# Kernel tuning notes

Measured on AMD Instinct MI355X. Metric: run time of the kernel, lower is better.

The kernel has to match this reference:

```python
import jax, jax.numpy as jnp
import numpy as np

B, T, V, E, D = 64, 512, 512, 128, 256


def setup_inputs() -> dict:
    key = jax.random.key(0)
    ks = jax.random.split(key, 9)
    g = lambda k, sh, s: jax.random.normal(k, sh, jnp.float32) * np.float32(s)
    return {
        "x": jax.random.randint(ks[0], (B, T), 0, V),
        "embed": g(ks[1], (V, E), 1.0),
        "W_ih": g(ks[2], (E, D), 1.0 / np.sqrt(E)),
        "W_hh": g(ks[3], (D, D), 1.0 / np.sqrt(D)),
        "b_h": jnp.zeros((D,), jnp.float32),
        "W_attn": g(ks[4], (D, D), 1.0 / np.sqrt(D)),
        "U_attn": g(ks[5], (D, D), 1.0 / np.sqrt(D)),
        "v_attn": g(ks[6], (D,), 1.0 / np.sqrt(D)),
        "fc_W": g(ks[7], (2 * D, V), 1.0 / np.sqrt(2 * D)),
        "fc_b": jnp.zeros((V,), jnp.float32),
    }


def _forward(x, embed, W_ih, W_hh, b_h, W_attn, U_attn, v_attn, fc_W, fc_b):
    Bn, Tn = x.shape
    Dn = W_hh.shape[0]
    # precompute input projection for every step: [T, B, D]
    xp = jnp.swapaxes(embed[x] @ W_ih + b_h, 0, 1)
    pos = jnp.arange(Tn)

    def step(carry, x_t):
        h_prev, Hbuf, Pbuf, t = carry  # Hbuf: past hidden states, Pbuf: W_attn-projected
        h = jnp.tanh(x_t + h_prev @ W_hh)  # [B, D]
        # Bahdanau attention over strictly-past states (slots < t)
        cur_proj = h @ U_attn  # [B, D]
        energy = jnp.einsum('tbd,d->tb', jnp.tanh(Pbuf + cur_proj[None]), v_attn)
        energy = jnp.where((pos < t)[:, None], energy, -1e9)
        w = jax.nn.softmax(energy, axis=0)  # [T, B]
        ctx = jnp.einsum('tb,tbd->bd', w, Hbuf)
        ctx = jnp.where(t == 0, h, ctx)  # first step: context = h itself
        logits = jnp.concatenate([h, ctx], axis=-1) @ fc_W + fc_b  # [B, V]
        Hbuf = Hbuf.at[t].set(h)
        Pbuf = Pbuf.at[t].set(h @ W_attn)
        return (h, Hbuf, Pbuf, t + 1), logits

    h0 = jnp.zeros((Bn, Dn), xp.dtype)
    buf = jnp.zeros((Tn, Bn, Dn), xp.dtype)
    _, outs = jax.lax.scan(step, (h0, buf, buf, jnp.asarray(0, jnp.int32)), xp)
    return jnp.swapaxes(outs, 0, 1)  # [B, T, V]


def reference(x, embed, W_ih, W_hh, b_h, W_attn, U_attn, v_attn, fc_W, fc_b):
    return _forward(x, embed, W_ih, W_hh, b_h, W_attn, U_attn, v_attn, fc_W, fc_b)
```

## Files before the change

kernel.cpp:

```cpp
#include <hip/hip_runtime.h>
#include <hip/hip_bf16.h>

#define B_  64
#define T_  512
#define V_  512
#define E_  128
#define D_  256
#define D2_ 512

typedef unsigned short u16;
typedef unsigned int   u32;
typedef short s16x8 __attribute__((ext_vector_type(8)));
typedef _Float16 f16x8 __attribute__((ext_vector_type(8)));
typedef float f32x4 __attribute__((ext_vector_type(4)));
typedef unsigned short u16x2 __attribute__((ext_vector_type(2)));
typedef unsigned short u16x4 __attribute__((ext_vector_type(4)));

__device__ __forceinline__ float bf2f(u16 u){
    union { u32 i; float f; } c; c.i = ((u32)u) << 16; return c.f;
}
__device__ __forceinline__ u16 f2bf(float f){
    union { float f; u32 i; } c; c.f = f;
    u32 u = c.i;
    return (u16)((u + 0x7fffu + ((u >> 16) & 1u)) >> 16);
}
__device__ __forceinline__ u16 f2h(float f){
    union { _Float16 h; u16 u; } c; c.h = (_Float16)f; return c.u;
}
__device__ __forceinline__ float tanh_b(float x){
    float e = __expf(2.0f * x);
    return fmaf(-2.0f, __builtin_amdgcn_rcpf(e + 1.0f), 1.0f);
}
__device__ __forceinline__ void barrier_lgkm(){
    asm volatile("s_waitcnt lgkmcnt(0)\n\ts_barrier" ::: "memory");
}

__global__ __launch_bounds__(256) void k_ew_cvt(const float* __restrict__ embed,
                                                const float* __restrict__ W_ih,
                                                const float* __restrict__ b_h,
                                                float* __restrict__ EW,
                                                const float* __restrict__ W_att,
                                                const float* __restrict__ U_att,
                                                const float* __restrict__ fc_W,
                                                u16* __restrict__ Wab,
                                                u16* __restrict__ Uab,
                                                u16* __restrict__ fcWb){
    __shared__ float er[E_];
    int blk = blockIdx.x;
    int tid = threadIdx.x;
    if (blk < V_){
        if (tid < E_) er[tid] = embed[blk*E_ + tid];
        __syncthreads();
        float acc = b_h[tid];
        #pragma unroll 4
        for (int e = 0; e < E_; ++e) acc += er[e] * W_ih[e*D_ + tid];
        EW[blk*D_ + tid] = acc;
    } else {
        int i = (blk - V_) * 256 + tid;
        if (i < 65536){
            int n = i >> 8, k = i & 255;
            Wab[i] = f2bf(W_att[k*D_ + n]);
        } else if (i < 131072){
            int j = i - 65536;
            int n = j >> 8, k = j & 255;
            Uab[j] = f2bf(U_att[k*D_ + n]);
        } else {
            int j = i - 131072;
            int n = j >> 9, k = j & 511;
            fcWb[j] = f2bf(fc_W[k*V_ + n]);
        }
    }
}

__global__ __launch_bounds__(256) void k_gather(const int* __restrict__ x,
                                                const float* __restrict__ EW,
                                                float* __restrict__ XP){
    int m = blockIdx.x * 4 + (threadIdx.x >> 6);
    int lane = threadIdx.x & 63;
    int b = m & 63, t = m >> 6;
    int v = x[b*T_ + t];
    float4 val = *(const float4*)&EW[v*D_ + lane*4];
    *(float4*)&XP[(size_t)m*D_ + lane*4] = val;
}

__global__ __launch_bounds__(512, 2) void k_rnn(const float* __restrict__ XP,
                                                const float* __restrict__ W_hh,
                                                u16* __restrict__ HC){
    __shared__ u16 hf[2][4][272];
    int tid  = threadIdx.x;
    int lane = tid & 63;
    int w    = tid >> 6;
    int col  = lane & 15;
    int colA = col & 3;
    int quad = lane >> 4;
    int bb0  = blockIdx.x * 4;

    f16x8 bfh[2][8];
    #pragma unroll
    for (int nt = 0; nt < 2; ++nt){
        int n = w*32 + nt*16 + col;
        #pragma unroll
        for (int ks = 0; ks < 8; ++ks){
            f16x8 th;
            #pragma unroll
            for (int j = 0; j < 8; ++j){
                int k = ks*32 + quad*8 + j;
                th[j] = (_Float16)W_hh[k*D_ + n];
            }
            bfh[nt][ks] = th;
        }
    }
    for (int i = tid; i < 2*4*272; i += 512) (&hf[0][0][0])[i] = 0;

    const float* p  = XP + (size_t)bb0*D_ + w*32 + col;
    u16*         hc = HC + (size_t)bb0*D2_ + w*32 + col;

    float ewv[2][4];
    #pragma unroll
    for (int nt = 0; nt < 2; ++nt)
        #pragma unroll
        for (int r = 0; r < 4; ++r)
            ewv[nt][r] = p[r*D_ + nt*16];
    p += (size_t)B_*D_;
    __syncthreads();

    for (int t = 0; t < T_; ++t){
        int rb = t & 1, wb = rb ^ 1;
        f32x4 acc[2];
        #pragma unroll
        for (int nt = 0; nt < 2; ++nt)
            #pragma unroll
            for (int r = 0; r < 4; ++r) acc[nt][r] = ewv[nt][r];

        f16x8 ah[8];
        #pragma unroll
        for (int ks = 0; ks < 8; ++ks)
            ah[ks] = *(const f16x8*)&hf[rb][colA][ks*32 + quad*8];

        if (t + 1 < T_){
            #pragma unroll
            for (int nt = 0; nt < 2; ++nt)
                #pragma unroll
                for (int r = 0; r < 4; ++r)
                    ewv[nt][r] = p[r*D_ + nt*16];
        }
        p += (size_t)B_*D_;

        #pragma unroll
        for (int ks = 0; ks < 8; ++ks){
            acc[0] = __builtin_amdgcn_mfma_f32_16x16x32_f16(ah[ks], bfh[0][ks], acc[0], 0, 0, 0);
            acc[1] = __builtin_amdgcn_mfma_f32_16x16x32_f16(ah[ks], bfh[1][ks], acc[1], 0, 0, 0);
        }

        #pragma unroll
        for (int nt = 0; nt < 2; ++nt){
            f32x4 s = acc[nt];
            float v = (quad & 2) ? ((quad & 1) ? s[3] : s[2])
                                 : ((quad & 1) ? s[1] : s[0]);
            float h  = tanh_b(v);
            int n    = w*32 + nt*16 + col;
            hf[wb][quad][n]      = f2h(h);
            hc[quad*D2_ + nt*16] = f2bf(h);
        }
        hc += (size_t)B_*D2_;
        barrier_lgkm();
    }
}

__global__ __launch_bounds__(256) void k_gemm(const u16* __restrict__ A, int lda,
                                              const u16* __restrict__ Wb,
                                              const float* __restrict__ bias,
                                              void* __restrict__ out,
                                              int K, int N, int mode){
    __shared__ u16 As[64][88];
    __shared__ u16 Ws[64][88];
    int tid  = threadIdx.x;
    int lane = tid & 63;
    int w    = tid >> 6;
    int col  = lane & 15;
    int quad = lane >> 4;
    int m0   = blockIdx.x * 64;
    int n0   = blockIdx.y * 64;

    f32x4 acc[4];
    #pragma unroll
    for (int nt = 0; nt < 4; ++nt)
        #pragma unroll
        for (int r = 0; r < 4; ++r) acc[nt][r] = 0.0f;

    for (int kk = 0; kk < K; kk += 64){
        #pragma unroll
        for (int i = 0; i < 2; ++i){
            int idx = tid + i*256;
            int r   = idx >> 3;
            int c8  = (idx & 7) * 8;
            *(s16x8*)&As[r][c8] = *(const s16x8*)&A [(size_t)(m0 + r)*lda + kk + c8];
            *(s16x8*)&Ws[r][c8] = *(const s16x8*)&Wb[(size_t)(n0 + r)*K   + kk + c8];
        }
        barrier_lgkm();
        #pragma unroll
        for (int ks = 0; ks < 2; ++ks){
            s16x8 a = *(const s16x8*)&As[w*16 + col][ks*32 + quad*8];
            #pragma unroll
            for (int nt = 0; nt < 4; ++nt){
                s16x8 b = *(const s16x8*)&Ws[nt*16 + col][ks*32 + quad*8];
                acc[nt] = __builtin_amdgcn_mfma_f32_16x16x32_bf16(a, b, acc[nt], 0, 0, 0);
            }
        }
        barrier_lgkm();
    }
    #pragma unroll
    for (int nt = 0; nt < 4; ++nt){
        int n = n0 + nt*16 + col;
        float bv = (mode == 1 && bias) ? bias[n] : 0.0f;
        #pragma unroll
        for (int r = 0; r < 4; ++r){
            int m = m0 + w*16 + quad*4 + r;
            float v = acc[nt][r] + bv;
            if (mode == 1){
                int b = m & 63, t = m >> 6;
                ((float*)out)[(size_t)(b*T_ + t)*V_ + n] = v;
            } else if (mode == 2){
                ((u16*)out)[(size_t)m*N + n] = f2bf(__expf(2.0f * v));
            } else if (mode == 3){
                u16* dst = (u16*)out + ((size_t)(n >> 8)) * ((size_t)32768 * 256);
                dst[(size_t)m*256 + (n & 255)] = f2bf(__expf(2.0f * v));
            } else {
                ((u16*)out)[(size_t)m*N + n] = f2bf(v);
            }
        }
    }
}

__global__ __launch_bounds__(512) void k_fc(const u16* __restrict__ A,
                                            const u16* __restrict__ Wb,
                                            const float* __restrict__ bias,
                                            float* __restrict__ out){
    __shared__ u16 As[128][88];
    __shared__ u16 Ws[128][88];
    int tid  = threadIdx.x;
    int lane = tid & 63;
    int w    = tid >> 6;
    int wm   = w >> 2;
    int wn   = w & 3;
    int col  = lane & 15;
    int quad = lane >> 4;
    int m0   = blockIdx.x * 128;
    int n0   = blockIdx.y * 128;

    f32x4 acc[4][2];
    #pragma unroll
    for (int mt = 0; mt < 4; ++mt)
        #pragma unroll
        for (int nt = 0; nt < 2; ++nt)
            #pragma unroll
            for (int r = 0; r < 4; ++r) acc[mt][nt][r] = 0.0f;

    for (int kk = 0; kk < D2_; kk += 64){
        #pragma unroll
        for (int i = 0; i < 2; ++i){
            int idx = tid + i*512;
            int r   = idx >> 3;
            int c8  = (idx & 7) * 8;
            *(s16x8*)&As[r][c8] = *(const s16x8*)&A [(size_t)(m0 + r)*D2_ + kk + c8];
            *(s16x8*)&Ws[r][c8] = *(const s16x8*)&Wb[(size_t)(n0 + r)*D2_ + kk + c8];
        }
        barrier_lgkm();
        #pragma unroll
        for (int ks = 0; ks < 2; ++ks){
            s16x8 b0 = *(const s16x8*)&Ws[wn*32 +      col][ks*32 + quad*8];
            s16x8 b1 = *(const s16x8*)&Ws[wn*32 + 16 + col][ks*32 + quad*8];
            #pragma unroll
            for (int mt = 0; mt < 4; ++mt){
                s16x8 a = *(const s16x8*)&As[wm*64 + mt*16 + col][ks*32 + quad*8];
                acc[mt][0] = __builtin_amdgcn_mfma_f32_16x16x32_bf16(a, b0, acc[mt][0], 0, 0, 0);
                acc[mt][1] = __builtin_amdgcn_mfma_f32_16x16x32_bf16(a, b1, acc[mt][1], 0, 0, 0);
            }
        }
        barrier_lgkm();
    }
    #pragma unroll
    for (int nt = 0; nt < 2; ++nt){
        int n = n0 + wn*32 + nt*16 + col;
        float bv = bias[n];
        #pragma unroll
        for (int mt = 0; mt < 4; ++mt){
            #pragma unroll
            for (int r = 0; r < 4; ++r){
                int m = m0 + wm*64 + mt*16 + quad*4 + r;
                int b = m & 63, t = m >> 6;
                out[(size_t)(b*T_ + t)*V_ + n] = acc[mt][nt][r] + bv;
            }
        }
    }
}

__global__ __launch_bounds__(256) void k_energy(const u16* __restrict__ EP,
                                                const u16* __restrict__ EQ,
                                                const float* __restrict__ v_attn,
                                                u16* __restrict__ Wx){
    __shared__ float eps[32][288];
    int tid = threadIdx.x;
    int blk = blockIdx.x;
    int b   = blk / 136;
    int pi  = blk % 136;
    int tt  = 0;
    while ((tt+1)*(tt+2)/2 <= pi) ++tt;
    int pt  = pi - tt*(tt+1)/2;

    int t_l = tid >> 3;
    int dg  = tid & 7;
    int d0  = dg * 32;
    int t   = tt*32 + t_l;

    #pragma unroll
    for (int i = 0; i < 8; ++i){
        int idx = tid + i*256;
        int row = idx >> 6;
        int c4  = (idx & 63) * 4;
        int pc  = c4 + ((c4 >> 5) << 2);
        u16x4 v4 = *(const u16x4*)&EP[((size_t)((pt*32 + row)*B_ + b))*D_ + c4];
        float4 f4 = make_float4(bf2f(v4.x), bf2f(v4.y), bf2f(v4.z), bf2f(v4.w));
        *(float4*)&eps[row][pc] = f4;
    }

    float eq[32], vm2[32], sv = 0.0f;
    #pragma unroll
    for (int i = 0; i < 8; ++i){
        u16x4 v4 = *(const u16x4*)&EQ[((size_t)(t*B_ + b))*D_ + d0 + i*4];
        eq[i*4+0] = bf2f(v4.x); eq[i*4+1] = bf2f(v4.y);
        eq[i*4+2] = bf2f(v4.z); eq[i*4+3] = bf2f(v4.w);
    }
    #pragma unroll
    for (int i = 0; i < 32; ++i){
        float v = v_attn[d0 + i];
        sv += v;
        vm2[i] = -2.0f * v;
    }
    barrier_lgkm();

    for (int tpl = 0; tpl < 32; ++tpl){
        int tp = pt*32 + tpl;
        float acc = sv;
        #pragma unroll
        for (int g = 0; g < 8; ++g){
            float4 ep = *(const float4*)&eps[tpl][dg*36 + 4*g];
            float da = fmaf(ep.x, eq[4*g+0], 1.0f);
            float db = fmaf(ep.y, eq[4*g+1], 1.0f);
            float dc = fmaf(ep.z, eq[4*g+2], 1.0f);
            float dd = fmaf(ep.w, eq[4*g+3], 1.0f);
            float dab = da * db;
            float dcd = dc * dd;
            float nab = fmaf(vm2[4*g+1], da, vm2[4*g+0] * db);
            float ncd = fmaf(vm2[4*g+3], dc, vm2[4*g+2] * dd);
            float num = fmaf(ncd, dab, nab * dcd);
            acc = fmaf(num, __builtin_amdgcn_rcpf(dab * dcd), acc);
        }
        acc += __shfl_xor(acc, 1);
        acc += __shfl_xor(acc, 2);
        acc += __shfl_xor(acc, 4);
        if (dg == 0 && tp < t){
            Wx[((size_t)(b*T_ + t))*T_ + tp] = f2bf(__expf(acc));
        }
    }
}

__global__ __launch_bounds__(256) void k_ctx(const u16* __restrict__ Wx,
                                             u16* __restrict__ HC){
    __shared__ u16 As[64][88];
    __shared__ u16 Ws[64][88];
    __shared__ float rs[64];
    int tid  = threadIdx.x;
    int lane = tid & 63;
    int w    = tid >> 6;
    int col  = lane & 15;
    int quad = lane >> 4;
    int b    = blockIdx.y;
    int m0   = (blockIdx.x >> 2) * 64;
    int n0   = (blockIdx.x & 3) * 64;

    const u16* A = Wx + (size_t)b * T_ * T_;

    int r0 = tid >> 3;
    int c8 = (tid & 7) * 8;
    float rsum0 = 0.0f, rsum1 = 0.0f;

    f32x4 acc[4];
    #pragma unroll
    for (int nt = 0; nt < 4; ++nt)
        #pragma unroll
        for (int r = 0; r < 4; ++r) acc[nt][r] = 0.0f;

    int kmax = m0 + 64;
    for (int kk = 0; kk < kmax; kk += 64){
        bool diag = (kk == m0);
        #pragma unroll
        for (int i = 0; i < 2; ++i){
            int r = r0 + i*32;
            s16x8 v = *(const s16x8*)&A[(size_t)(m0 + r)*T_ + kk + c8];
            if (diag){
                #pragma unroll
                for (int j = 0; j < 8; ++j)
                    if (c8 + j >= r) v[j] = 0;
            }
            *(s16x8*)&As[r][c8] = v;
            float s = 0.0f;
            #pragma unroll
            for (int j = 0; j < 8; ++j) s += bf2f((u16)v[j]);
            if (i == 0) rsum0 += s; else rsum1 += s;
        }
        #pragma unroll
        for (int i = 0; i < 8; ++i){
            int idx = tid + i*256;
            int k   = idx >> 5;
            int n2  = (idx & 31) * 2;
            u16x2 v2 = *(const u16x2*)&HC[((size_t)((kk + k)*B_ + b))*D2_ + n0 + n2];
            Ws[n2][k]   = v2.x;
            Ws[n2+1][k] = v2.y;
        }
        barrier_lgkm();
        #pragma unroll
        for (int ks = 0; ks < 2; ++ks){
            s16x8 a = *(const s16x8*)&As[w*16 + col][ks*32 + quad*8];
            #pragma unroll
            for (int nt = 0; nt < 4; ++nt){
                s16x8 bb = *(const s16x8*)&Ws[nt*16 + col][ks*32 + quad*8];
                acc[nt] = __builtin_amdgcn_mfma_f32_16x16x32_bf16(a, bb, acc[nt], 0, 0, 0);
            }
        }
        barrier_lgkm();
    }

    rsum0 += __shfl_xor(rsum0, 1); rsum0 += __shfl_xor(rsum0, 2); rsum0 += __shfl_xor(rsum0, 4);
    rsum1 += __shfl_xor(rsum1, 1); rsum1 += __shfl_xor(rsum1, 2); rsum1 += __shfl_xor(rsum1, 4);
    if ((tid & 7) == 0){ rs[r0] = rsum0; rs[r0 + 32] = rsum1; }
    barrier_lgkm();

    float linv[4];
    #pragma unroll
    for (int r = 0; r < 4; ++r){
        int rr = w*16 + quad*4 + r;
        float lv = (m0 + rr > 0) ? rs[rr] : 1.0f;
        linv[r] = 1.0f / lv;
    }
    #pragma unroll
    for (int nt = 0; nt < 4; ++nt){
        int n = n0 + nt*16 + col;
        #pragma unroll
        for (int r = 0; r < 4; ++r){
            int t = m0 + w*16 + quad*4 + r;
            u16 ov;
            if (t == 0) ov = HC[(size_t)b*D2_ + n];
            else        ov = f2bf(acc[nt][r] * linv[r]);
            HC[((size_t)(t*B_ + b))*D2_ + D_ + n] = ov;
        }
    }
}

extern "C" void kernel_launch(void* const* d_in, const int* in_sizes, int n_in,
                              void* d_out, int out_size, void* d_ws, size_t ws_size,
                              hipStream_t stream){
    const int*   x     = (const int*)d_in[0];
    const float* embed = (const float*)d_in[1];
    const float* W_ih  = (const float*)d_in[2];
    const float* W_hh  = (const float*)d_in[3];
    const float* b_h   = (const float*)d_in[4];
    const float* W_att = (const float*)d_in[5];
    const float* U_att = (const float*)d_in[6];
    const float* v_att = (const float*)d_in[7];
    const float* fc_W  = (const float*)d_in[8];
    const float* fc_b  = (const float*)d_in[9];

    char* ws = (char*)d_ws;
    float* EW   = (float*)ws;
    u16*   Wab  = (u16*)(ws + 524288);
    u16*   Uab  = (u16*)(ws + 655360);
    u16*   fcWb = (u16*)(ws + 786432);
    u16*   HC   = (u16*)(ws + 1310720);
    u16*   EP   = (u16*)(ws + 34865152);
    u16*   EQ   = (u16*)(ws + 51642368);
    float* XP   = (float*)(ws + 34865152);
    u16*   Wx   = (u16*)d_out;

    k_ew_cvt<<<dim3(2048),        dim3(256), 0, stream>>>(embed, W_ih, b_h, EW,
                                                          W_att, U_att, fc_W,
                                                          Wab, Uab, fcWb);
    k_gather<<<dim3(T_*B_/4),     dim3(256), 0, stream>>>(x, EW, XP);
    k_rnn   <<<dim3(16),          dim3(512), 0, stream>>>(XP, W_hh, HC);
    k_gemm  <<<dim3(512, 8),      dim3(256), 0, stream>>>(HC, D2_, Wab, nullptr, (void*)EP, D_, D2_, 3);
    k_energy<<<dim3(B_*136),      dim3(256), 0, stream>>>(EP, EQ, v_att, Wx);
    k_ctx   <<<dim3(32, B_),      dim3(256), 0, stream>>>(Wx, HC);
    k_fc    <<<dim3(256, 4),      dim3(512), 0, stream>>>(HC, fcWb, fc_b, (float*)d_out);
}
```

Before: 686.0 us.

## Fuse RNN, projection GEMM and energy into persistent mega-kernel with flag sync

The separate RNN, projection GEMM and energy kernels are merged into one persistent kernel. Sixteen blocks run the recurrence and publish progress flags every 8 timesteps. The remaining blocks pull work items from an atomic queue, spin-wait on those flags, and then compute P/Q projection tiles and energy tiles while the serial RNN is still running. The aim is to hide the GEMM and energy work behind the latency-bound recurrence. The cost is spin-wait overhead, reliance on all blocks being co-resident to avoid deadlock, and a workspace/output buffer layout reshuffled to hold the flags.

```diff
diff --git a/kernel.cpp b/kernel.cpp
--- a/kernel.cpp
+++ b/kernel.cpp
@@ -7,6 +7,10 @@
 #define E_  128
 #define D_  256
 #define D2_ 512
+
+#define NPQ    4096
+#define NEN    8704
+#define NITEMS (NPQ + NEN)
 
 typedef unsigned short u16;
 typedef unsigned int   u32;
@@ -41,10 +45,7 @@
                                                 float* __restrict__ EW,
                                                 const float* __restrict__ W_att,
                                                 const float* __restrict__ U_att,
-                                                const float* __restrict__ fc_W,
-                                                u16* __restrict__ Wab,
-                                                u16* __restrict__ Uab,
-                                                u16* __restrict__ fcWb){
+                                                u16* __restrict__ Wab){
     __shared__ float er[E_];
     int blk = blockIdx.x;
     int tid = threadIdx.x;
@@ -60,14 +61,10 @@
         if (i < 65536){
             int n = i >> 8, k = i & 255;
             Wab[i] = f2bf(W_att[k*D_ + n]);
-        } else if (i < 131072){
+        } else {
             int j = i - 65536;
             int n = j >> 8, k = j & 255;
-            Uab[j] = f2bf(U_att[k*D_ + n]);
-        } else {
-            int j = i - 131072;
-            int n = j >> 9, k = j & 511;
-            fcWb[j] = f2bf(fc_W[k*V_ + n]);
+            Wab[i] = f2bf(U_att[k*D_ + n]);
         }
     }
 }
@@ -83,11 +80,20 @@
     *(float4*)&XP[(size_t)m*D_ + lane*4] = val;
 }
 
-__global__ __launch_bounds__(512, 2) void k_rnn(const float* __restrict__ XP,
-                                                const float* __restrict__ W_hh,
-                                                u16* __restrict__ HC){
-    __shared__ u16 hf[2][4][272];
-    int tid  = threadIdx.x;
+__global__ __launch_bounds__(256) void k_cvt_fc(const float* __restrict__ fc_W,
+                                                u16* __restrict__ fcWb){
+    int j = blockIdx.x * 256 + threadIdx.x;
+    int n = j >> 9, k = j & 511;
+    fcWb[j] = f2bf(fc_W[k*V_ + n]);
+}
+
+
+__device__ void rnn_block(const float* __restrict__ XP,
+                          const float* __restrict__ W_hh,
+                          u16* __restrict__ HC,
+                          u32* __restrict__ flags,
+                          char* smem, int tid){
+    u16 (*hf)[4][272] = (u16 (*)[4][272])smem;
     int lane = tid & 63;
     int w    = tid >> 6;
     int col  = lane & 15;
@@ -163,24 +169,214 @@
             hc[quad*D2_ + nt*16] = f2bf(h);
         }
         hc += (size_t)B_*D2_;
+
+        if ((t & 7) == 7){
+            asm volatile("s_waitcnt vmcnt(0) lgkmcnt(0)" ::: "memory");
+            __syncthreads();
+            if (tid == 0)
+                __hip_atomic_fetch_add(&flags[t >> 3], 1u,
+                                       __ATOMIC_RELEASE, __HIP_MEMORY_SCOPE_AGENT);
+        } else {
+            barrier_lgkm();
+        }
+    }
+}
+
+__device__ void pq_tile(int t, int nt, const u16* __restrict__ HC,
+                        const u16* __restrict__ Wab,
+                        u16* __restrict__ EP, u16* __restrict__ EQ,
+                        char* smem, int tid){
+    u16 (*As)[88] = (u16 (*)[88])smem;
+    u16 (*Ws)[88] = (u16 (*)[88])(smem + 64*88*2);
+    int lane = tid & 63;
+    int w  = tid >> 6;
+    int wm = w >> 2, wn = w & 3;
+    int col = lane & 15, quad = lane >> 4;
+    int m0 = t * 64, n0 = nt * 64;
+    int r  = tid >> 3, c8 = (tid & 7) * 8;
+
+    f32x4 acc[2];
+    #pragma unroll
+    for (int mt = 0; mt < 2; ++mt)
+        #pragma unroll
+        for (int rr = 0; rr < 4; ++rr) acc[mt][rr] = 0.0f;
+
+    for (int kk = 0; kk < D_; kk += 64){
+        *(s16x8*)&As[r][c8] = *(const s16x8*)&HC [(size_t)(m0 + r)*D2_ + kk + c8];
+        *(s16x8*)&Ws[r][c8] = *(const s16x8*)&Wab[(size_t)(n0 + r)*D_  + kk + c8];
         barrier_lgkm();
-    }
-}
-
-__global__ __launch_bounds__(256) void k_gemm(const u16* __restrict__ A, int lda,
-                                              const u16* __restrict__ Wb,
-                                              const float* __restrict__ bias,
-                                              void* __restrict__ out,
-                                              int K, int N, int mode){
+        #pragma unroll
+        for (int ks = 0; ks < 2; ++ks){
+            s16x8 b = *(const s16x8*)&Ws[wn*16 + col][ks*32 + quad*8];
+            #pragma unroll
+            for (int mt = 0; mt < 2; ++mt){
+                s16x8 a = *(const s16x8*)&As[wm*32 + mt*16 + col][ks*32 + quad*8];
+                acc[mt] = __builtin_amdgcn_mfma_f32_16x16x32_bf16(a, b, acc[mt], 0, 0, 0);
+            }
+        }
+        barrier_lgkm();
+    }
+    int n = n0 + wn*16 + col;
+    u16* dst = (n < D_) ? EP : EQ;
+    int nn = n & 255;
+    #pragma unroll
+    for (int mt = 0; mt < 2; ++mt)
+        #pragma unroll
+        for (int rr = 0; rr < 4; ++rr){
+            int m = m0 + wm*32 + mt*16 + quad*4 + rr;
+            dst[(size_t)m*D_ + nn] = f2bf(__expf(2.0f * acc[mt][rr]));
+        }
+}
+
+__device__ void energy_tile(int b, int tt, int pt,
+                            const u16* __restrict__ EP, const u16* __restrict__ EQ,
+                            const float* __restrict__ v_attn,
+                            u16* __restrict__ Wx, char* smem, int tid){
+    float (*eps)[288] = (float (*)[288])smem;
+    int tg = tid >> 4, dg = tid & 15;
+    int d0 = dg * 16;
+    int t  = tt*32 + tg;
+
+    #pragma unroll
+    for (int i = 0; i < 4; ++i){
+        int idx = tid + i*512;
+        int row = idx >> 6;
+        int c4  = (idx & 63) * 4;
+        int pc  = c4 + ((c4 >> 5) << 2);
+        u16x4 v4 = *(const u16x4*)&EP[((size_t)((pt*32 + row)*B_ + b))*D_ + c4];
+        *(float4*)&eps[row][pc] = make_float4(bf2f(v4.x), bf2f(v4.y), bf2f(v4.z), bf2f(v4.w));
+    }
+
+    float eq[16], vm2[16], sv = 0.0f;
+    #pragma unroll
+    for (int i = 0; i < 4; ++i){
+        u16x4 v4 = *(const u16x4*)&EQ[((size_t)(t*B_ + b))*D_ + d0 + i*4];
+        eq[i*4+0] = bf2f(v4.x); eq[i*4+1] = bf2f(v4.y);
+        eq[i*4+2] = bf2f(v4.z); eq[i*4+3] = bf2f(v4.w);
+    }
+    #pragma unroll
+    for (int i = 0; i < 16; ++i){
+        float v = v_attn[d0 + i];
+        sv += v;
+        vm2[i] = -2.0f * v;
+    }
+    int po[4];
+    #pragma unroll
+    for (int g = 0; g < 4; ++g){ int c = d0 + 4*g; po[g] = c + ((c >> 5) << 2); }
+    barrier_lgkm();
+
+    for (int tpl = 0; tpl < 32; ++tpl){
+        int tp = pt*32 + tpl;
+        float acc = sv;
+        #pragma unroll
+        for (int g = 0; g < 4; ++g){
+            float4 ep = *(const float4*)&eps[tpl][po[g]];
+            float da = fmaf(ep.x, eq[4*g+0], 1.0f);
+            float db = fmaf(ep.y, eq[4*g+1], 1.0f);
+            float dc = fmaf(ep.z, eq[4*g+2], 1.0f);
+            float dd = fmaf(ep.w, eq[4*g+3], 1.0f);
+            float dab = da * db;
+            float dcd = dc * dd;
+            float nab = fmaf(vm2[4*g+1], da, vm2[4*g+0] * db);
+            float ncd = fmaf(vm2[4*g+3], dc, vm2[4*g+2] * dd);
+            float num = fmaf(ncd, dab, nab * dcd);
+            acc = fmaf(num, __builtin_amdgcn_rcpf(dab * dcd), acc);
+        }
+        acc += __shfl_xor(acc, 1);
+        acc += __shfl_xor(acc, 2);
+        acc += __shfl_xor(acc, 4);
+        acc += __shfl_xor(acc, 8);
+        if (dg == 0 && tp < t)
+            Wx[((size_t)(b*T_ + t))*T_ + tp] = f2bf(__expf(acc));
+    }
+}
+
+__device__ void worker_loop(const u16* __restrict__ HC,
+                            const u16* __restrict__ Wab,
+                            u16* __restrict__ EP, u16* __restrict__ EQ,
+                            const float* __restrict__ v_attn,
+                            u16* __restrict__ Wx,
+                            u32* __restrict__ flags,
+                            char* smem, int tid){
+    volatile int* s_item = (volatile int*)(smem + 36864);
+    for (;;){
+        __syncthreads();
+        if (tid == 0)
+            *s_item = (int)__hip_atomic_fetch_add(&flags[95], 1u,
+                          __ATOMIC_RELAXED, __HIP_MEMORY_SCOPE_AGENT);
+        __syncthreads();
+        int item = *s_item;
+        if (item >= NITEMS) return;
+
+        if (item < NPQ){
+            int t  = item >> 3, nt = item & 7;
+            if (tid == 0){
+                while (__hip_atomic_load(&flags[t >> 3], __ATOMIC_ACQUIRE,
+                                         __HIP_MEMORY_SCOPE_AGENT) < 16u)
+                    __builtin_amdgcn_s_sleep(8);
+            }
+            __syncthreads();
+            pq_tile(t, nt, HC, Wab, EP, EQ, smem, tid);
+            asm volatile("s_waitcnt vmcnt(0)" ::: "memory");
+            __syncthreads();
+            if (tid == 0)
+                __hip_atomic_fetch_add(&flags[64 + (t >> 5)], 1u,
+                                       __ATOMIC_RELEASE, __HIP_MEMORY_SCOPE_AGENT);
+        } else {
+            int e  = item - NPQ;
+            int pi = e >> 6, b = e & 63;
+            int tt = 0;
+            while ((tt+1)*(tt+2)/2 <= pi) ++tt;
+            int pt = pi - tt*(tt+1)/2;
+            if (tid == 0){
+                while (__hip_atomic_load(&flags[64 + tt], __ATOMIC_ACQUIRE,
+                                         __HIP_MEMORY_SCOPE_AGENT) < 256u)
+                    __builtin_amdgcn_s_sleep(8);
+                while (__hip_atomic_load(&flags[64 + pt], __ATOMIC_ACQUIRE,
+                                         __HIP_MEMORY_SCOPE_AGENT) < 256u)
+                    __builtin_amdgcn_s_sleep(8);
+            }
+            __syncthreads();
+            energy_tile(b, tt, pt, EP, EQ, v_attn, Wx, smem, tid);
+        }
+    }
+}
+
+__global__ __launch_bounds__(512, 2) void k_mega(const float* __restrict__ XP,
+                                                 const float* __restrict__ W_hh,
+                                                 u16* __restrict__ HC,
+                                                 const u16* __restrict__ Wab,
+                                                 const float* __restrict__ v_attn,
+                                                 u16* __restrict__ EP,
+                                                 u16* __restrict__ EQ,
+                                                 u16* __restrict__ Wx,
+                                                 u32* __restrict__ flags){
+    __shared__ __align__(16) char smem[36880];
+    int tid = threadIdx.x;
+    if (blockIdx.x < 16)
+        rnn_block(XP, W_hh, HC, flags, smem, tid);
+    worker_loop(HC, Wab, EP, EQ, v_attn, Wx, flags, smem, tid);
+}
+
+__global__ __launch_bounds__(256) void k_ctx(const u16* __restrict__ Wx,
+                                             u16* __restrict__ HC){
     __shared__ u16 As[64][88];
     __shared__ u16 Ws[64][88];
+    __shared__ float rs[64];
     int tid  = threadIdx.x;
     int lane = tid & 63;
     int w    = tid >> 6;
     int col  = lane & 15;
     int quad = lane >> 4;
-    int m0   = blockIdx.x * 64;
-    int n0   = blockIdx.y * 64;
+    int b    = blockIdx.y;
+    int m0   = (blockIdx.x >> 2) * 64;
+    int n0   = (blockIdx.x & 3) * 64;
+
+    const u16* A = Wx + (size_t)b * T_ * T_;
+
+    int r0 = tid >> 3;
+    int c8 = (tid & 7) * 8;
+    float rsum0 = 0.0f, rsum1 = 0.0f;
 
     f32x4 acc[4];
     #pragma unroll
@@ -188,14 +384,32 @@
         #pragma unroll
         for (int r = 0; r < 4; ++r) acc[nt][r] = 0.0f;
 
-    for (int kk = 0; kk < K; kk += 64){
+    int kmax = m0 + 64;
+    for (int kk = 0; kk < kmax; kk += 64){
+        bool diag = (kk == m0);
         #pragma unroll
         for (int i = 0; i < 2; ++i){
+            int r = r0 + i*32;
+            s16x8 v = *(const s16x8*)&A[(size_t)(m0 + r)*T_ + kk + c8];
+            if (diag){
+                #pragma unroll
+                for (int j = 0; j < 8; ++j)
+                    if (c8 + j >= r) v[j] = 0;
+            }
+            *(s16x8*)&As[r][c8] = v;
+            float s = 0.0f;
+            #pragma unroll
+            for (int j = 0; j < 8; ++j) s += bf2f((u16)v[j]);
+            if (i == 0) rsum0 += s; else rsum1 += s;
+        }
+        #pragma unroll
+        for (int i = 0; i < 8; ++i){
             int idx = tid + i*256;
-            int r   = idx >> 3;
-            int c8  = (idx & 7) * 8;
-            *(s16x8*)&As[r][c8] = *(const s16x8*)&A [(size_t)(m0 + r)*lda + kk + c8];
-            *(s16x8*)&Ws[r][c8] = *(const s16x8*)&Wb[(size_t)(n0 + r)*K   + kk + c8];
+            int k   = idx >> 5;
+            int n2  = (idx & 31) * 2;
+            u16x2 v2 = *(const u16x2*)&HC[((size_t)((kk + k)*B_ + b))*D2_ + n0 + n2];
+            Ws[n2][k]   = v2.x;
+            Ws[n2+1][k] = v2.y;
         }
         barrier_lgkm();
         #pragma unroll
@@ -203,31 +417,35 @@
             s16x8 a = *(const s16x8*)&As[w*16 + col][ks*32 + quad*8];
             #pragma unroll
             for (int nt = 0; nt < 4; ++nt){
-                s16x8 b = *(const s16x8*)&Ws[nt*16 + col][ks*32 + quad*8];
-                acc[nt] = __builtin_amdgcn_mfma_f32_16x16x32_bf16(a, b, acc[nt], 0, 0, 0);
+                s16x8 bb = *(const s16x8*)&Ws[nt*16 + col][ks*32 + quad*8];
+                acc[nt] = __builtin_amdgcn_mfma_f32_16x16x32_bf16(a, bb, acc[nt], 0, 0, 0);
             }
         }
         barrier_lgkm();
+    }
+
+    rsum0 += __shfl_xor(rsum0, 1); rsum0 += __shfl_xor(rsum0, 2); rsum0 += __shfl_xor(rsum0, 4);
+    rsum1 += __shfl_xor(rsum1, 1); rsum1 += __shfl_xor(rsum1, 2); rsum1 += __shfl_xor(rsum1, 4);
+    if ((tid & 7) == 0){ rs[r0] = rsum0; rs[r0 + 32] = rsum1; }
+    barrier_lgkm();
+
+    float linv[4];
+    #pragma unroll
+    for (int r = 0; r < 4; ++r){
+        int rr = w*16 + quad*4 + r;
+        float lv = (m0 + rr > 0) ? rs[rr] : 1.0f;
+        linv[r] = 1.0f / lv;
     }
     #pragma unroll
     for (int nt = 0; nt < 4; ++nt){
         int n = n0 + nt*16 + col;
-        float bv = (mode == 1 && bias) ? bias[n] : 0.0f;
         #pragma unroll
         for (int r = 0; r < 4; ++r){
-            int m = m0 + w*16 + quad*4 + r;
-            float v = acc[nt][r] + bv;
-            if (mode == 1){
-                int b = m & 63, t = m >> 6;
-                ((float*)out)[(size_t)(b*T_ + t)*V_ + n] = v;
-            } else if (mode == 2){
-                ((u16*)out)[(size_t)m*N + n] = f2bf(__expf(2.0f * v));
-            } else if (mode == 3){
-                u16* dst = (u16*)out + ((size_t)(n >> 8)) * ((size_t)32768 * 256);
-                dst[(size_t)m*256 + (n & 255)] = f2bf(__expf(2.0f * v));
-            } else {
-                ((u16*)out)[(size_t)m*N + n] = f2bf(v);
-            }
+            int t = m0 + w*16 + quad*4 + r;
+            u16 ov;
+            if (t == 0) ov = HC[(size_t)b*D2_ + n];
+            else        ov = f2bf(acc[nt][r] * linv[r]);
+            HC[((size_t)(t*B_ + b))*D2_ + D_ + n] = ov;
         }
     }
 }
@@ -295,168 +513,6 @@
     }
 }
 
-__global__ __launch_bounds__(256) void k_energy(const u16* __restrict__ EP,
-                                                const u16* __restrict__ EQ,
-                                                const float* __restrict__ v_attn,
-                                                u16* __restrict__ Wx){
-    __shared__ float eps[32][288];
-    int tid = threadIdx.x;
-    int blk = blockIdx.x;
-    int b   = blk / 136;
-    int pi  = blk % 136;
-    int tt  = 0;
-    while ((tt+1)*(tt+2)/2 <= pi) ++tt;
-    int pt  = pi - tt*(tt+1)/2;
-
-    int t_l = tid >> 3;
-    int dg  = tid & 7;
-    int d0  = dg * 32;
-    int t   = tt*32 + t_l;
-
-    #pragma unroll
-    for (int i = 0; i < 8; ++i){
-        int idx = tid + i*256;
-        int row = idx >> 6;
-        int c4  = (idx & 63) * 4;
-        int pc  = c4 + ((c4 >> 5) << 2);
-        u16x4 v4 = *(const u16x4*)&EP[((size_t)((pt*32 + row)*B_ + b))*D_ + c4];
-        float4 f4 = make_float4(bf2f(v4.x), bf2f(v4.y), bf2f(v4.z), bf2f(v4.w));
-        *(float4*)&eps[row][pc] = f4;
-    }
-
-    float eq[32], vm2[32], sv = 0.0f;
-    #pragma unroll
-    for (int i = 0; i < 8; ++i){
-        u16x4 v4 = *(const u16x4*)&EQ[((size_t)(t*B_ + b))*D_ + d0 + i*4];
-        eq[i*4+0] = bf2f(v4.x); eq[i*4+1] = bf2f(v4.y);
-        eq[i*4+2] = bf2f(v4.z); eq[i*4+3] = bf2f(v4.w);
-    }
-    #pragma unroll
-    for (int i = 0; i < 32; ++i){
-        float v = v_attn[d0 + i];
-        sv += v;
-        vm2[i] = -2.0f * v;
-    }
-    barrier_lgkm();
-
-    for (int tpl = 0; tpl < 32; ++tpl){
-        int tp = pt*32 + tpl;
-        float acc = sv;
-        #pragma unroll
-        for (int g = 0; g < 8; ++g){
-            float4 ep = *(const float4*)&eps[tpl][dg*36 + 4*g];
-            float da = fmaf(ep.x, eq[4*g+0], 1.0f);
-            float db = fmaf(ep.y, eq[4*g+1], 1.0f);
-            float dc = fmaf(ep.z, eq[4*g+2], 1.0f);
-            float dd = fmaf(ep.w, eq[4*g+3], 1.0f);
-            float dab = da * db;
-            float dcd = dc * dd;
-            float nab = fmaf(vm2[4*g+1], da, vm2[4*g+0] * db);
-            float ncd = fmaf(vm2[4*g+3], dc, vm2[4*g+2] * dd);
-            float num = fmaf(ncd, dab, nab * dcd);
-            acc = fmaf(num, __builtin_amdgcn_rcpf(dab * dcd), acc);
-        }
-        acc += __shfl_xor(acc, 1);
-        acc += __shfl_xor(acc, 2);
-        acc += __shfl_xor(acc, 4);
-        if (dg == 0 && tp < t){
-            Wx[((size_t)(b*T_ + t))*T_ + tp] = f2bf(__expf(acc));
-        }
-    }
-}
-
-__global__ __launch_bounds__(256) void k_ctx(const u16* __restrict__ Wx,
-                                             u16* __restrict__ HC){
-    __shared__ u16 As[64][88];
-    __shared__ u16 Ws[64][88];
-    __shared__ float rs[64];
-    int tid  = threadIdx.x;
-    int lane = tid & 63;
-    int w    = tid >> 6;
-    int col  = lane & 15;
-    int quad = lane >> 4;
-    int b    = blockIdx.y;
-    int m0   = (blockIdx.x >> 2) * 64;
-    int n0   = (blockIdx.x & 3) * 64;
-
-    const u16* A = Wx + (size_t)b * T_ * T_;
-
-    int r0 = tid >> 3;
-    int c8 = (tid & 7) * 8;
-    float rsum0 = 0.0f, rsum1 = 0.0f;
-
-    f32x4 acc[4];
-    #pragma unroll
-    for (int nt = 0; nt < 4; ++nt)
-        #pragma unroll
-        for (int r = 0; r < 4; ++r) acc[nt][r] = 0.0f;
-
-    int kmax = m0 + 64;
-    for (int kk = 0; kk < kmax; kk += 64){
-        bool diag = (kk == m0);
-        #pragma unroll
-        for (int i = 0; i < 2; ++i){
-            int r = r0 + i*32;
-            s16x8 v = *(const s16x8*)&A[(size_t)(m0 + r)*T_ + kk + c8];
-            if (diag){
-                #pragma unroll
-                for (int j = 0; j < 8; ++j)
-                    if (c8 + j >= r) v[j] = 0;
-            }
-            *(s16x8*)&As[r][c8] = v;
-            float s = 0.0f;
-            #pragma unroll
-            for (int j = 0; j < 8; ++j) s += bf2f((u16)v[j]);
-            if (i == 0) rsum0 += s; else rsum1 += s;
-        }
-        #pragma unroll
-        for (int i = 0; i < 8; ++i){
-            int idx = tid + i*256;
-            int k   = idx >> 5;
-            int n2  = (idx & 31) * 2;
-            u16x2 v2 = *(const u16x2*)&HC[((size_t)((kk + k)*B_ + b))*D2_ + n0 + n2];
-            Ws[n2][k]   = v2.x;
-            Ws[n2+1][k] = v2.y;
-        }
-        barrier_lgkm();
-        #pragma unroll
-        for (int ks = 0; ks < 2; ++ks){
-            s16x8 a = *(const s16x8*)&As[w*16 + col][ks*32 + quad*8];
-            #pragma unroll
-            for (int nt = 0; nt < 4; ++nt){
-                s16x8 bb = *(const s16x8*)&Ws[nt*16 + col][ks*32 + quad*8];
-                acc[nt] = __builtin_amdgcn_mfma_f32_16x16x32_bf16(a, bb, acc[nt], 0, 0, 0);
-            }
-        }
-        barrier_lgkm();
-    }
-
-    rsum0 += __shfl_xor(rsum0, 1); rsum0 += __shfl_xor(rsum0, 2); rsum0 += __shfl_xor(rsum0, 4);
-    rsum1 += __shfl_xor(rsum1, 1); rsum1 += __shfl_xor(rsum1, 2); rsum1 += __shfl_xor(rsum1, 4);
-    if ((tid & 7) == 0){ rs[r0] = rsum0; rs[r0 + 32] = rsum1; }
-    barrier_lgkm();
-
-    float linv[4];
-    #pragma unroll
-    for (int r = 0; r < 4; ++r){
-        int rr = w*16 + quad*4 + r;
-        float lv = (m0 + rr > 0) ? rs[rr] : 1.0f;
-        linv[r] = 1.0f / lv;
-    }
-    #pragma unroll
-    for (int nt = 0; nt < 4; ++nt){
-        int n = n0 + nt*16 + col;
-        #pragma unroll
-        for (int r = 0; r < 4; ++r){
-            int t = m0 + w*16 + quad*4 + r;
-            u16 ov;
-            if (t == 0) ov = HC[(size_t)b*D2_ + n];
-            else        ov = f2bf(acc[nt][r] * linv[r]);
-            HC[((size_t)(t*B_ + b))*D2_ + D_ + n] = ov;
-        }
-    }
-}
-
 extern "C" void kernel_launch(void* const* d_in, const int* in_sizes, int n_in,
                               void* d_out, int out_size, void* d_ws, size_t ws_size,
                               hipStream_t stream){
@@ -473,22 +529,25 @@
 
     char* ws = (char*)d_ws;
     float* EW   = (float*)ws;
+    u16*   fcWb = (u16*)ws;
     u16*   Wab  = (u16*)(ws + 524288);
-    u16*   Uab  = (u16*)(ws + 655360);
-    u16*   fcWb = (u16*)(ws + 786432);
-    u16*   HC   = (u16*)(ws + 1310720);
-    u16*   EP   = (u16*)(ws + 34865152);
-    u16*   EQ   = (u16*)(ws + 51642368);
-    float* XP   = (float*)(ws + 34865152);
-    u16*   Wx   = (u16*)d_out;
-
-    k_ew_cvt<<<dim3(2048),        dim3(256), 0, stream>>>(embed, W_ih, b_h, EW,
-                                                          W_att, U_att, fc_W,
-                                                          Wab, Uab, fcWb);
-    k_gather<<<dim3(T_*B_/4),     dim3(256), 0, stream>>>(x, EW, XP);
-    k_rnn   <<<dim3(16),          dim3(512), 0, stream>>>(XP, W_hh, HC);
-    k_gemm  <<<dim3(512, 8),      dim3(256), 0, stream>>>(HC, D2_, Wab, nullptr, (void*)EP, D_, D2_, 3);
-    k_energy<<<dim3(B_*136),      dim3(256), 0, stream>>>(EP, EQ, v_att, Wx);
-    k_ctx   <<<dim3(32, B_),      dim3(256), 0, stream>>>(Wx, HC);
-    k_fc    <<<dim3(256, 4),      dim3(512), 0, stream>>>(HC, fcWb, fc_b, (float*)d_out);
-}
+    u16*   HC   = (u16*)(ws + 786432);
+    float* XP   = (float*)(ws + 34340864);
+    u32*   flags= (u32*)(ws + 67895296);
+
+    char* dob = (char*)d_out;
+    u16*   Wx   = (u16*)dob;
+    u16*   EP   = (u16*)(dob + 33554432);
+    u16*   EQ   = (u16*)(dob + 50331648);
+
+    (void)hipMemsetAsync(flags, 0, 512, stream);
+
+    k_ew_cvt<<<dim3(1024),     dim3(256), 0, stream>>>(embed, W_ih, b_h, EW,
+                                                       W_att, U_att, Wab);
+    k_gather<<<dim3(T_*B_/4),  dim3(256), 0, stream>>>(x, EW, XP);
+    k_cvt_fc<<<dim3(1024),     dim3(256), 0, stream>>>(fc_W, fcWb);
+    k_mega  <<<dim3(256),      dim3(512), 0, stream>>>(XP, W_hh, HC, Wab, v_att,
+                                                       EP, EQ, Wx, flags);
+    k_ctx   <<<dim3(32, B_),   dim3(256), 0, stream>>>(Wx, HC);
+    k_fc    <<<dim3(256, 4),   dim3(512), 0, stream>>>(HC, fcWb, fc_b, (float*)d_out);
+}
```

Measured after the change: 1.809 ms. +163.7%, slower.
